# Performance work log

Hardware: AMD Instinct MI355X
Metric: run time of the kernel (lower is better)

Reference implementation:

```python
import jax, jax.numpy as jnp
import numpy as np

N, C, NELL, NSPEC = 4096, 128, 9, 10
K3, K2, K1 = 4, 2, 1
IRREPS_OUT = (("0e", 1), ("1o", 3))  # keep_irrep_out dims


def setup_inputs() -> dict:
    key = jax.random.key(0)
    ks = iter(jax.random.split(key, 32))

    def rn(shape, scale=1.0):
        return jax.random.normal(next(ks), shape, jnp.float32) * jnp.float32(scale)

    inp = {}
    inp["x"] = rn((N, C, NELL))
    inp["node_specie"] = jax.random.randint(next(ks), (N,), 0, NSPEC)
    for name, d in IRREPS_OUT:
        # CG symmetric-product basis tensors (fixed buffers), normalized per order
        inp[f"U3_{name}"] = rn((d, NELL, NELL, NELL, K3), 1.0 / np.sqrt(NELL ** 3))
        inp[f"U2_{name}"] = rn((d, NELL, NELL, K2), 1.0 / np.sqrt(NELL ** 2))
        inp[f"U1_{name}"] = rn((d, NELL, K1), 1.0 / np.sqrt(NELL))
        # per-species path-mixing weights, 'element' gradient normalization ~ 1/sqrt(k)
        inp[f"W3_{name}"] = rn((NSPEC, K3, C), 1.0 / np.sqrt(K3))
        inp[f"W2_{name}"] = rn((NSPEC, K2, C), 1.0 / np.sqrt(K2))
        inp[f"W1_{name}"] = rn((NSPEC, K1, C), 1.0 / np.sqrt(K1))
    inp["Wlin_0e"] = rn((C, C))
    inp["Wlin_1o"] = rn((C, C))
    inp["bias_0e"] = rn((C,), 0.1)
    return inp


def _symmetric_contraction(x, specie, U3, U2, U1, W3, W2, W1):
    # MACE iterative contraction: out = U3.W3.x; then (U2.W2 + out).x; then (U1.W1 + out).x
    w3, w2, w1 = W3[specie], W2[specie], W1[specie]  # (N, k, C)
    out = jnp.einsum("opqik,bkc,bci->bcopq", U3, w3, x)   # (N, C, d, 9, 9)
    c = jnp.einsum("opik,bkc->bcopi", U2, w2) + out
    out = jnp.einsum("bcopi,bci->bcop", c, x)             # (N, C, d, 9)
    c = jnp.einsum("oik,bkc->bcoi", U1, w1) + out
    out = jnp.einsum("bcoi,bci->bco", c, x)               # (N, C, d)
    return out


def reference(x, node_specie,
              U3_0e, U2_0e, U1_0e, W3_0e, W2_0e, W1_0e,
              U3_1o, U2_1o, U1_1o, W3_1o, W2_1o, W1_1o,
              Wlin_0e, Wlin_1o, bias_0e):
    n = x.shape[0]
    f0 = _symmetric_contraction(x, node_specie, U3_0e, U2_0e, U1_0e, W3_0e, W2_0e, W1_0e)  # (N, C, 1)
    f1 = _symmetric_contraction(x, node_specie, U3_1o, U2_1o, U1_1o, W3_1o, W2_1o, W1_1o)  # (N, C, 3)
    scale = jnp.float32(1.0 / np.sqrt(C))  # e3nn Linear path normalization
    y0 = jnp.einsum("nco,cm->nmo", f0, Wlin_0e) * scale + bias_0e[None, :, None]  # bias only on 0e
    y1 = jnp.einsum("nco,cm->nmo", f1, Wlin_1o) * scale
    # axis_to_mul: flatten (channels, ir_dim) per irrep and concatenate
    return jnp.concatenate([y0.reshape(n, -1), y1.reshape(n, -1)], axis=-1)  # (N, 128*1 + 128*3)
```

## Files before the change

### kernel.cpp

```cpp
#include <hip/hip_runtime.h>

#define N_NODES 4096
#define C_CH    128
#define NSPEC   10
#define NCUB    165
#define NQUAD   45
#define NMONO   219
#define NBLK    1280
#define NTILE   8

#define WS_CNT    0
#define WS_LIST   256
#define WS_U3SYM  164096
#define WS_U2SYM  174656
#define WS_F      176096

__global__ __launch_bounds__(256) void k_prep(
        const float* __restrict__ U3_0e, const float* __restrict__ U3_1o,
        const float* __restrict__ U2_0e, const float* __restrict__ U2_1o,
        const int* __restrict__ specie, int* __restrict__ cnt,
        int* __restrict__ list, float* __restrict__ U3sym,
        float* __restrict__ U2sym) {
    int blk = blockIdx.x;
    int t   = threadIdx.x;

    if (blk == 8) {
        __shared__ int scnt[NSPEC];
        if (t < NSPEC) scnt[t] = 0;
        __syncthreads();
        for (int i = t; i < N_NODES; i += 256) {
            int s = specie[i];
            int pos = atomicAdd(&scnt[s], 1);
            list[s * N_NODES + pos] = i;
        }
        __syncthreads();
        if (t < NSPEC) cnt[t] = scnt[t];
        return;
    }

    __shared__ unsigned char ta[NCUB], tb[NCUB], td[NCUB], qa[NQUAD], qb[NQUAD];
    if (t < NCUB) {
        int idx = 0, a = 0, b = 0, d = 0;
        for (int a0 = 0; a0 < 9; a0++)
            for (int b0 = a0; b0 < 9; b0++)
                for (int d0 = b0; d0 < 9; d0++) {
                    if (idx == t) { a = a0; b = b0; d = d0; }
                    idx++;
                }
        ta[t] = a; tb[t] = b; td[t] = d;
    } else if (t >= NCUB && t < NCUB + NQUAD) {
        int q = t - NCUB, idx = 0, a = 0, b = 0;
        for (int a0 = 0; a0 < 9; a0++)
            for (int b0 = a0; b0 < 9; b0++) { if (idx == q) { a = a0; b = b0; } idx++; }
        qa[q] = a; qb[q] = b;
    }
    __syncthreads();

    for (int task = blk * 256 + t; task < 2640 + 360; task += 8 * 256) {
        if (task < 2640) {
            int og = task / 660;
            int r  = task - og * 660;
            int m  = r >> 2, k = r & 3;
            int a = ta[m], b = tb[m], d = td[m];
            const float* U3 = (og == 0) ? U3_0e : U3_1o;
            int o = (og == 0) ? 0 : og - 1;
            const float* Ub = U3 + (size_t)o * 2916;
            #define U3AT(p,q,i) Ub[((p)*9+(q))*36 + (i)*4 + k]
            float sum = U3AT(a,b,d) + U3AT(a,d,b) + U3AT(b,a,d)
                      + U3AT(b,d,a) + U3AT(d,a,b) + U3AT(d,b,a);
            #undef U3AT
            float sc = (a == b && b == d) ? (1.f/6.f)
                     : ((a == b || b == d || a == d) ? 0.5f : 1.f);
            U3sym[(og * 165 + m) * 4 + k] = sum * sc;
        } else {
            int t2 = task - 2640;
            int og = t2 / 90;
            int r  = t2 - og * 90;
            int q  = r >> 1, k = r & 1;
            int a = qa[q], b = qb[q];
            const float* U2 = (og == 0) ? U2_0e : U2_1o;
            int o = (og == 0) ? 0 : og - 1;
            const float* Ub = U2 + (size_t)o * 162;
            float sum = Ub[(a*9 + b)*2 + k] + Ub[(b*9 + a)*2 + k];
            if (a == b) sum *= 0.5f;
            U2sym[(og * 45 + q) * 2 + k] = sum;
        }
    }
}

__global__ __launch_bounds__(256) void k_main(const float* __restrict__ x,
        const int* __restrict__ cnt, const int* __restrict__ list,
        const float* __restrict__ U3sym, const float* __restrict__ U2sym,
        const float* __restrict__ U1_0e, const float* __restrict__ U1_1o,
        const float* __restrict__ W3_0e, const float* __restrict__ W3_1o,
        const float* __restrict__ W2_0e, const float* __restrict__ W2_1o,
        const float* __restrict__ W1_0e, const float* __restrict__ W1_1o,
        float* __restrict__ fout) {
    __shared__ float  cfs[NMONO * 4];
    __shared__ float2 xsh[9 * 256];
    int bx   = blockIdx.x;
    int tile = bx / NBLK;
    int blk  = bx - tile * NBLK;
    int s = blk >> 7, c = blk & 127;
    int n = cnt[s];
    if (tile * 512 >= n) return;

    int tid = threadIdx.x;

    for (int e = tid; e < NMONO * 4; e += 256) {
        int m = e >> 2, og = e & 3;
        float val;
        if (m < NCUB) {
            const float* W3 = (og == 0) ? W3_0e : W3_1o;
            const float* u  = U3sym + (og * 165 + m) * 4;
            val = u[0] * W3[s*512 +       c] + u[1] * W3[s*512 + 128 + c]
                + u[2] * W3[s*512 + 256 + c] + u[3] * W3[s*512 + 384 + c];
        } else if (m < NCUB + NQUAD) {
            int q = m - NCUB;
            const float* W2 = (og == 0) ? W2_0e : W2_1o;
            const float* u  = U2sym + (og * 45 + q) * 2;
            val = u[0] * W2[s*256 + c] + u[1] * W2[s*256 + 128 + c];
        } else {
            int l = m - (NCUB + NQUAD);
            const float* U1 = (og == 0) ? U1_0e : U1_1o;
            const float* W1 = (og == 0) ? W1_0e : W1_1o;
            int o = (og == 0) ? 0 : og - 1;
            val = U1[o * 9 + l] * W1[s * 128 + c];
        }
        cfs[e] = val;
    }

    const int* __restrict__ lst = list + s * N_NODES;
    int i0 = tile * 512 + tid;
    int i1 = i0 + 256;
    int b0 = lst[i0 < n ? i0 : 0];
    int b1 = lst[i1 < n ? i1 : 0];
    const float* xp0 = x + ((size_t)b0 * C_CH + c) * 9;
    const float* xp1 = x + ((size_t)b1 * C_CH + c) * 9;
    #pragma unroll
    for (int i = 0; i < 9; i++)
        xsh[i * 256 + tid] = make_float2(xp0[i], xp1[i]);
    __syncthreads();

    float a0[4] = {0.f, 0.f, 0.f, 0.f};
    float a1[4] = {0.f, 0.f, 0.f, 0.f};
    int mcub = 0, mquad = 0;

    #pragma unroll 1
    for (int a = 0; a < 9; a++) {
        float2 xa = xsh[a * 256 + tid];
        {
            float4 cl = *(const float4*)&cfs[(210 + a) * 4];
            a0[0] = fmaf(cl.x, xa.x, a0[0]);  a1[0] = fmaf(cl.x, xa.y, a1[0]);
            a0[1] = fmaf(cl.y, xa.x, a0[1]);  a1[1] = fmaf(cl.y, xa.y, a1[1]);
            a0[2] = fmaf(cl.z, xa.x, a0[2]);  a1[2] = fmaf(cl.z, xa.y, a1[2]);
            a0[3] = fmaf(cl.w, xa.x, a0[3]);  a1[3] = fmaf(cl.w, xa.y, a1[3]);
        }
        #pragma unroll 1
        for (int b = a; b < 9; b++) {
            float2 xb = xsh[b * 256 + tid];
            float p0 = xa.x * xb.x, p1 = xa.y * xb.y;
            {
                float4 cq = *(const float4*)&cfs[(165 + mquad) * 4]; mquad++;
                a0[0] = fmaf(cq.x, p0, a0[0]);  a1[0] = fmaf(cq.x, p1, a1[0]);
                a0[1] = fmaf(cq.y, p0, a0[1]);  a1[1] = fmaf(cq.y, p1, a1[1]);
                a0[2] = fmaf(cq.z, p0, a0[2]);  a1[2] = fmaf(cq.z, p1, a1[2]);
                a0[3] = fmaf(cq.w, p0, a0[3]);  a1[3] = fmaf(cq.w, p1, a1[3]);
            }
            #pragma unroll 1
            for (int d = b; d < 9; d++) {
                float2 xd = xsh[d * 256 + tid];
                float4 c3 = *(const float4*)&cfs[mcub * 4]; mcub++;
                float q0 = p0 * xd.x, q1 = p1 * xd.y;
                a0[0] = fmaf(c3.x, q0, a0[0]);  a1[0] = fmaf(c3.x, q1, a1[0]);
                a0[1] = fmaf(c3.y, q0, a0[1]);  a1[1] = fmaf(c3.y, q1, a1[1]);
                a0[2] = fmaf(c3.z, q0, a0[2]);  a1[2] = fmaf(c3.z, q1, a1[2]);
                a0[3] = fmaf(c3.w, q0, a0[3]);  a1[3] = fmaf(c3.w, q1, a1[3]);
            }
        }
    }
    if (i0 < n) *(float4*)&fout[((size_t)b0 * C_CH + c) * 4] = make_float4(a0[0], a0[1], a0[2], a0[3]);
    if (i1 < n) *(float4*)&fout[((size_t)b1 * C_CH + c) * 4] = make_float4(a1[0], a1[1], a1[2], a1[3]);
}

__global__ __launch_bounds__(256) void k_epi(const float* __restrict__ f,
        const float* __restrict__ W0, const float* __restrict__ W1,
        const float* __restrict__ bias, float* __restrict__ out) {
    __shared__ float smem[128 * 65];
    int bx = blockIdx.x;
    int ntile = bx >> 3, jg = bx & 7;
    int n0 = ntile * 64;
    int t  = threadIdx.x;
    int o  = jg >> 1;

    #pragma unroll
    for (int r = 0; r < 32; ++r) {
        int flat = r * 256 + t;
        int n = flat >> 7, c = flat & 127;
        smem[c * 65 + n] = f[(size_t)(n0 + n) * 512 + c * 4 + o];
    }
    __syncthreads();

    int w    = __builtin_amdgcn_readfirstlane((int)(t >> 6));
    int lane = t & 63;
    int mb   = (jg & 1) * 64 + w * 16;
    const float* __restrict__ Wsel = (o == 0) ? W0 : W1;

    float acc[16];
    #pragma unroll
    for (int jj = 0; jj < 16; jj++) acc[jj] = 0.f;

    #pragma unroll 4
    for (int c = 0; c < 128; ++c) {
        float fv = smem[c * 65 + lane];
        #pragma unroll
        for (int jj = 0; jj < 16; jj++)
            acc[jj] = fmaf(fv, Wsel[c * 128 + mb + jj], acc[jj]);
    }
    __syncthreads();

    const float scale = 0.08838834764831845f;
    #pragma unroll
    for (int jj = 0; jj < 16; jj++) {
        float v = acc[jj] * scale;
        if (o == 0) v += bias[mb + jj];
        smem[(w * 16 + jj) * 65 + lane] = v;
    }
    __syncthreads();

    #pragma unroll
    for (int r = 0; r < 16; ++r) {
        int flat = r * 256 + t;
        int jl = flat & 63, n = flat >> 6;
        int m  = (jg & 1) * 64 + jl;
        int col = (o == 0) ? m : (128 + m * 3 + (o - 1));
        out[(size_t)(n0 + n) * 512 + col] = smem[jl * 65 + n];
    }
}

extern "C" void kernel_launch(void* const* d_in, const int* in_sizes, int n_in,
                              void* d_out, int out_size, void* d_ws, size_t ws_size,
                              hipStream_t stream) {
    const float* x     = (const float*)d_in[0];
    const int*   spec  = (const int*)  d_in[1];
    const float* U3_0e = (const float*)d_in[2];
    const float* U2_0e = (const float*)d_in[3];
    const float* U1_0e = (const float*)d_in[4];
    const float* W3_0e = (const float*)d_in[5];
    const float* W2_0e = (const float*)d_in[6];
    const float* W1_0e = (const float*)d_in[7];
    const float* U3_1o = (const float*)d_in[8];
    const float* U2_1o = (const float*)d_in[9];
    const float* U1_1o = (const float*)d_in[10];
    const float* W3_1o = (const float*)d_in[11];
    const float* W2_1o = (const float*)d_in[12];
    const float* W1_1o = (const float*)d_in[13];
    const float* Wlin0 = (const float*)d_in[14];
    const float* Wlin1 = (const float*)d_in[15];
    const float* bias0 = (const float*)d_in[16];
    float* out = (float*)d_out;

    char* ws = (char*)d_ws;
    int*   cnt   = (int*)  (ws + WS_CNT);
    int*   list  = (int*)  (ws + WS_LIST);
    float* U3sym = (float*)(ws + WS_U3SYM);
    float* U2sym = (float*)(ws + WS_U2SYM);
    float* f     = (float*)(ws + WS_F);
    (void)in_sizes; (void)n_in; (void)out_size; (void)ws_size;

    hipLaunchKernelGGL(k_prep, dim3(9), dim3(256), 0, stream,
                       U3_0e, U3_1o, U2_0e, U2_1o, spec, cnt, list, U3sym, U2sym);
    hipLaunchKernelGGL(k_main, dim3(NBLK * NTILE), dim3(256), 0, stream,
                       x, cnt, list, U3sym, U2sym, U1_0e, U1_1o,
                       W3_0e, W3_1o, W2_0e, W2_1o, W1_0e, W1_1o, f);
    hipLaunchKernelGGL(k_epi, dim3(512), dim3(256), 0, stream,
                       f, Wlin0, Wlin1, bias0, out);
}
```

Before: 165.2 us.

## Keep x in registers and fully unroll symmetric contraction with paced LDS reads

The main contraction kernel now loads each thread's two 9-element x vectors straight into registers instead of staging them in shared memory, and fully unrolls the cubic/quadratic/linear monomial loops with compile-time indices. Scheduling barriers interleave one LDS coefficient read with eight FMAs so loads and math overlap. This removes shared-memory traffic for x and the loop overhead, at the cost of higher register pressure and larger code. A sync is added after the coefficient fill.

```diff
diff --git a/kernel.cpp b/kernel.cpp
--- a/kernel.cpp
+++ b/kernel.cpp
@@ -96,8 +96,7 @@
         const float* __restrict__ W2_0e, const float* __restrict__ W2_1o,
         const float* __restrict__ W1_0e, const float* __restrict__ W1_1o,
         float* __restrict__ fout) {
-    __shared__ float  cfs[NMONO * 4];
-    __shared__ float2 xsh[9 * 256];
+    __shared__ float4 cfs4[NMONO];
     int bx   = blockIdx.x;
     int tile = bx / NBLK;
     int blk  = bx - tile * NBLK;
@@ -107,6 +106,7 @@
 
     int tid = threadIdx.x;
 
+    float* cfs = (float*)cfs4;
     for (int e = tid; e < NMONO * 4; e += 256) {
         int m = e >> 2, og = e & 3;
         float val;
@@ -129,6 +129,7 @@
         }
         cfs[e] = val;
     }
+    __syncthreads();
 
     const int* __restrict__ lst = list + s * N_NODES;
     int i0 = tile * 512 + tid;
@@ -137,50 +138,50 @@
     int b1 = lst[i1 < n ? i1 : 0];
     const float* xp0 = x + ((size_t)b0 * C_CH + c) * 9;
     const float* xp1 = x + ((size_t)b1 * C_CH + c) * 9;
-    #pragma unroll
-    for (int i = 0; i < 9; i++)
-        xsh[i * 256 + tid] = make_float2(xp0[i], xp1[i]);
-    __syncthreads();
-
-    float a0[4] = {0.f, 0.f, 0.f, 0.f};
-    float a1[4] = {0.f, 0.f, 0.f, 0.f};
-    int mcub = 0, mquad = 0;
-
-    #pragma unroll 1
+    float x0[9], x1[9];
+    #pragma unroll
+    for (int i = 0; i < 9; i++) { x0[i] = xp0[i]; x1[i] = xp1[i]; }
+
+    float4 a0 = make_float4(0.f, 0.f, 0.f, 0.f);
+    float4 a1 = make_float4(0.f, 0.f, 0.f, 0.f);
+    int m3 = 0, m2 = 0;
+
+    #define FMA4(acc, cf, xv) \
+        acc.x = fmaf(cf.x, xv, acc.x); acc.y = fmaf(cf.y, xv, acc.y); \
+        acc.z = fmaf(cf.z, xv, acc.z); acc.w = fmaf(cf.w, xv, acc.w);
+    #define PACE() \
+        __builtin_amdgcn_sched_group_barrier(0x100, 1, 0); \
+        __builtin_amdgcn_sched_group_barrier(0x002, 8, 0);
+
+    #pragma unroll
     for (int a = 0; a < 9; a++) {
-        float2 xa = xsh[a * 256 + tid];
         {
-            float4 cl = *(const float4*)&cfs[(210 + a) * 4];
-            a0[0] = fmaf(cl.x, xa.x, a0[0]);  a1[0] = fmaf(cl.x, xa.y, a1[0]);
-            a0[1] = fmaf(cl.y, xa.x, a0[1]);  a1[1] = fmaf(cl.y, xa.y, a1[1]);
-            a0[2] = fmaf(cl.z, xa.x, a0[2]);  a1[2] = fmaf(cl.z, xa.y, a1[2]);
-            a0[3] = fmaf(cl.w, xa.x, a0[3]);  a1[3] = fmaf(cl.w, xa.y, a1[3]);
-        }
-        #pragma unroll 1
+            float4 cl = cfs4[210 + a];
+            FMA4(a0, cl, x0[a])  FMA4(a1, cl, x1[a])
+            PACE()
+        }
+        #pragma unroll
         for (int b = a; b < 9; b++) {
-            float2 xb = xsh[b * 256 + tid];
-            float p0 = xa.x * xb.x, p1 = xa.y * xb.y;
+            float p0 = x0[a] * x0[b], p1 = x1[a] * x1[b];
             {
-                float4 cq = *(const float4*)&cfs[(165 + mquad) * 4]; mquad++;
-                a0[0] = fmaf(cq.x, p0, a0[0]);  a1[0] = fmaf(cq.x, p1, a1[0]);
-                a0[1] = fmaf(cq.y, p0, a0[1]);  a1[1] = fmaf(cq.y, p1, a1[1]);
-                a0[2] = fmaf(cq.z, p0, a0[2]);  a1[2] = fmaf(cq.z, p1, a1[2]);
-                a0[3] = fmaf(cq.w, p0, a0[3]);  a1[3] = fmaf(cq.w, p1, a1[3]);
+                float4 cq = cfs4[165 + m2]; m2++;
+                FMA4(a0, cq, p0)  FMA4(a1, cq, p1)
+                PACE()
             }
-            #pragma unroll 1
+            #pragma unroll
             for (int d = b; d < 9; d++) {
-                float2 xd = xsh[d * 256 + tid];
-                float4 c3 = *(const float4*)&cfs[mcub * 4]; mcub++;
-                float q0 = p0 * xd.x, q1 = p1 * xd.y;
-                a0[0] = fmaf(c3.x, q0, a0[0]);  a1[0] = fmaf(c3.x, q1, a1[0]);
-                a0[1] = fmaf(c3.y, q0, a0[1]);  a1[1] = fmaf(c3.y, q1, a1[1]);
-                a0[2] = fmaf(c3.z, q0, a0[2]);  a1[2] = fmaf(c3.z, q1, a1[2]);
-                a0[3] = fmaf(c3.w, q0, a0[3]);  a1[3] = fmaf(c3.w, q1, a1[3]);
+                float4 c3 = cfs4[m3]; m3++;
+                float q0 = p0 * x0[d], q1 = p1 * x1[d];
+                FMA4(a0, c3, q0)  FMA4(a1, c3, q1)
+                PACE()
             }
         }
     }
-    if (i0 < n) *(float4*)&fout[((size_t)b0 * C_CH + c) * 4] = make_float4(a0[0], a0[1], a0[2], a0[3]);
-    if (i1 < n) *(float4*)&fout[((size_t)b1 * C_CH + c) * 4] = make_float4(a1[0], a1[1], a1[2], a1[3]);
+    #undef PACE
+    #undef FMA4
+
+    if (i0 < n) *(float4*)&fout[((size_t)b0 * C_CH + c) * 4] = a0;
+    if (i1 < n) *(float4*)&fout[((size_t)b1 * C_CH + c) * 4] = a1;
 }
 
 __global__ __launch_bounds__(256) void k_epi(const float* __restrict__ f,
```

New measurement: 527.7 us. 3.19x slower.
